# Optimization experiments

Hardware: AMD Instinct MI355X
Metric: run time of the kernel (lower is better)

Reference implementation:

```python
import jax, jax.numpy as jnp
import numpy as np

B, T, E, NH = 2, 1024, 512, 8


def setup_inputs() -> dict:
    key = jax.random.key(0)
    ks = jax.random.split(key, 7)
    s = 0.02
    return {
        "x": jax.random.normal(ks[0], (B, T, E), dtype=jnp.float32),
        "W_qkv": jax.random.normal(ks[1], (E, 3 * E), dtype=jnp.float32) * s,
        "b_qkv": jax.random.normal(ks[2], (3 * E,), dtype=jnp.float32) * s,
        "W_od": jax.random.normal(ks[3], (E, 2 * NH), dtype=jnp.float32) * s,
        "b_od": jax.random.normal(ks[4], (2 * NH,), dtype=jnp.float32) * s,
        "W_out": jax.random.normal(ks[5], (E, E), dtype=jnp.float32) * s,
        "b_out": jax.random.normal(ks[6], (E,), dtype=jnp.float32) * s,
        "length": T,
    }


def reference(x, W_qkv, b_qkv, W_od, b_od, W_out, b_out, length):
    b, t, e = x.shape
    nh = W_od.shape[1] // 2
    hd = e // nh
    scaling = float(hd) ** (-0.5)

    qkv = x @ W_qkv + b_qkv
    Q, K, V = jnp.split(qkv, 3, axis=-1)  # each (b, t, e)

    od = Q @ W_od + b_od  # (b, t, 2*nh)
    offset, duration = jnp.split(od, 2, axis=-1)
    offset = jnp.tanh(offset) * length
    duration = jax.nn.sigmoid(duration) * length

    qidx = jnp.arange(length, dtype=x.dtype)[None, :, None]  # (1, t, 1)
    anchor = qidx + offset  # (b, t, nh)

    # 'b t nh -> (b nh) t'
    anchor = anchor.transpose(0, 2, 1).reshape(b * nh, t)
    duration = duration.transpose(0, 2, 1).reshape(b * nh, t)

    start = anchor - duration
    end = anchor + duration
    bl = jnp.floor(start)          # left bound index
    br = jnp.ceil(end)             # right bound index
    al = jnp.floor(anchor)         # anchor left index
    ar = al + 1                    # anchor right index
    dist_al = anchor - al          # anchor_dist_l

    r = jnp.arange(length, dtype=x.dtype)[None, None, :]  # (1, 1, t)

    def pmask(idx):  # point mask (bnh, t, t), float
        return (r == idx[:, :, None]).astype(x.dtype)

    point_weight = (1.0
                    + (bl - start)[:, :, None] * pmask(bl)
                    + (end - br)[:, :, None] * pmask(br)
                    + dist_al[:, :, None] * pmask(ar)
                    + (1.0 - dist_al)[:, :, None] * pmask(al))

    attn_mask = (r < bl[:, :, None]) | (r > br[:, :, None])  # (bnh, t, t) bool

    def heads(z):  # 'b t (nh hd) -> (b nh) t hd'
        return z.reshape(b, t, nh, hd).transpose(0, 2, 1, 3).reshape(b * nh, t, hd)

    Qh, Kh, Vh = heads(Q), heads(K), heads(V)

    scores = jnp.einsum('bic,brc->bir', Qh, Kh) * scaling
    scores = scores * point_weight
    scores = jnp.where(attn_mask, jnp.asarray(-1e8, x.dtype), scores)
    attn = jax.nn.softmax(scores, axis=-1)

    out = jnp.einsum('bir,brc->bic', attn, Vh)  # (bnh, t, hd)
    out = out.reshape(b, nh, t, hd).transpose(0, 2, 1, 3).reshape(b, t, e)
    return out @ W_out + b_out
```

## Files before the change

kernel.cpp:

```cpp
#include <hip/hip_runtime.h>

typedef unsigned short ushort_t;
typedef short s16x8 __attribute__((ext_vector_type(8)));
typedef float f32x4 __attribute__((ext_vector_type(4)));

#define DEVINL __device__ __forceinline__

DEVINL ushort_t f2b(float f) {
  union { float f; unsigned int u; } v; v.f = f;
  unsigned int r = (v.u + 0x7fffu + ((v.u >> 16) & 1u)) >> 16;
  return (ushort_t)r;
}

DEVINL ushort_t f2b_hw(float f) {
  union { __bf16 h; ushort_t u; } cv;
  cv.h = (__bf16)f;
  return cv.u;
}

__global__ __launch_bounds__(256) void prep_kernel(
    const float* __restrict__ Wqkv, const float* __restrict__ bq,
    const float* __restrict__ Wod, const float* __restrict__ bod,
    const float* __restrict__ Wout,
    ushort_t* __restrict__ WqkvT, ushort_t* __restrict__ WoT,
    float* __restrict__ Wcomb, float* __restrict__ bcomb)
{
  __shared__ ushort_t tile[64 * 72];
  const int b = blockIdx.x;
  const int tid = threadIdx.x;

  if (b < 256) {
    const float* in;
    ushort_t* out;
    int N, bx, by;
    if (b < 192) { in = Wqkv; out = WqkvT; N = 1536; bx = b % 24; by = b / 24; }
    else         { in = Wout; out = WoT;   N = 512;  bx = (b - 192) % 8; by = (b - 192) / 8; }
    const int K = 512;
    const int n0 = bx * 64, k0 = by * 64;
    const int cr = tid >> 4;
    const int cc = (tid & 15) * 4;
#pragma unroll
    for (int p = 0; p < 4; p++) {
      int k = k0 + p * 16 + cr;
      float4 v = *(const float4*)(in + k * N + n0 + cc);
      ushort4 o; o.x = f2b(v.x); o.y = f2b(v.y); o.z = f2b(v.z); o.w = f2b(v.w);
      *(ushort4*)(tile + (p * 16 + cr) * 72 + cc) = o;
    }
    __syncthreads();
#pragma unroll
    for (int p = 0; p < 4; p++) {
      int n = n0 + p * 16 + cr;
      ushort4 v;
      v.x = tile[(cc + 0) * 72 + p * 16 + cr];
      v.y = tile[(cc + 1) * 72 + p * 16 + cr];
      v.z = tile[(cc + 2) * 72 + p * 16 + cr];
      v.w = tile[(cc + 3) * 72 + p * 16 + cr];
      *(ushort4*)(out + n * K + k0 + cc) = v;
    }
    return;
  }

  const int w = tid >> 6, lane = tid & 63;
  const int c = (b - 256) * 4 + w;
  if (c > 512) return;
  float a[8];
  const float* src = (c < 512) ? (Wqkv + c * 1536 + lane * 8) : (bq + lane * 8);
  float4 a0 = *(const float4*)(src);
  float4 a1 = *(const float4*)(src + 4);
  a[0]=a0.x; a[1]=a0.y; a[2]=a0.z; a[3]=a0.w;
  a[4]=a1.x; a[5]=a1.y; a[6]=a1.z; a[7]=a1.w;

  float s[16];
#pragma unroll
  for (int j = 0; j < 16; j++) s[j] = 0.f;
#pragma unroll
  for (int i = 0; i < 8; i++) {
    const float* wp = Wod + (lane * 8 + i) * 16;
#pragma unroll
    for (int j = 0; j < 16; j++) s[j] += a[i] * wp[j];
  }
#pragma unroll
  for (int mask = 1; mask < 64; mask <<= 1)
#pragma unroll
    for (int j = 0; j < 16; j++) s[j] += __shfl_xor(s[j], mask);

  if (lane < 16) {
    if (c < 512) Wcomb[c * 16 + lane] = s[lane];
    else         bcomb[lane] = s[lane] + bod[lane];
  }
}

__global__ __launch_bounds__(256) void od_kernel(
    const float* __restrict__ x, const float* __restrict__ Wcomb,
    const float* __restrict__ bcomb, const int* __restrict__ lenp,
    float* __restrict__ params, ushort_t* __restrict__ xb)
{
  const int w = threadIdx.x >> 6, lane = threadIdx.x & 63;
  const int m = blockIdx.x * 4 + w;
  int li = lenp[0];
  float len = (li > 0 && li < 1048576) ? (float)li : 1024.0f;

  const float* qp = x + m * 512 + lane * 8;
  float q[8];
  float4 qa = *(const float4*)(qp);
  float4 qb = *(const float4*)(qp + 4);
  q[0]=qa.x; q[1]=qa.y; q[2]=qa.z; q[3]=qa.w;
  q[4]=qb.x; q[5]=qb.y; q[6]=qb.z; q[7]=qb.w;

  s16x8 ov;
#pragma unroll
  for (int i = 0; i < 8; i++) ov[i] = (short)f2b(q[i]);
  *(s16x8*)(xb + m * 512 + lane * 8) = ov;

  float s[16];
#pragma unroll
  for (int j = 0; j < 16; j++) s[j] = 0.f;
#pragma unroll
  for (int i = 0; i < 8; i++) {
    const float* wp = Wcomb + (lane * 8 + i) * 16;
#pragma unroll
    for (int j = 0; j < 16; j++) s[j] += q[i] * wp[j];
  }
#pragma unroll
  for (int mask = 1; mask < 64; mask <<= 1)
#pragma unroll
    for (int j = 0; j < 16; j++) s[j] += __shfl_xor(s[j], mask);

  if (lane < 8) {
    int h = lane;
    int bb = m >> 10, t = m & 1023;
    float odo = s[h] + bcomb[h];
    float odd = s[8 + h] + bcomb[8 + h];
    float offset = tanhf(odo) * len;
    float dur = len / (1.f + expf(-odd));
    float anchor = (float)t + offset;
    float start = anchor - dur, end = anchor + dur;
    float bl = floorf(start), br = ceilf(end);
    float al = floorf(anchor);
    float da = anchor - al;
    float* pp = params + ((bb * 8 + h) * 1024 + t) * 6;
    pp[0] = bl; pp[1] = br; pp[2] = al;
    pp[3] = bl - start; pp[4] = end - br; pp[5] = da;
  }
}

__global__ __launch_bounds__(256) void qkv_gemm_kernel(
    const ushort_t* __restrict__ xb, const ushort_t* __restrict__ WT,
    const float* __restrict__ bqkv,
    ushort_t* __restrict__ Qh, ushort_t* __restrict__ Kh, ushort_t* __restrict__ VT)
{
  __shared__ ushort_t As[64 * 32];
  __shared__ ushort_t Bs[128 * 32];
  const int tid = threadIdx.x;
  const int lane = tid & 63, w = tid >> 6;
  const int wr = w >> 1, wc = w & 1;
  const int quad = lane >> 4, l16 = lane & 15;
  const int m0 = blockIdx.y * 64, n0 = blockIdx.x * 128;

  f32x4 acc[2][4];
#pragma unroll
  for (int i = 0; i < 2; i++)
#pragma unroll
    for (int j = 0; j < 4; j++) acc[i][j] = f32x4{0.f, 0.f, 0.f, 0.f};

  const int idx = tid * 8;
  const int ra = idx >> 5, ca = idx & 31;
  const int rb1 = (idx + 2048) >> 5, cb1 = (idx + 2048) & 31;

  for (int k0 = 0; k0 < 512; k0 += 32) {
    s16x8 va  = *(const s16x8*)(xb + (m0 + ra) * 512 + k0 + ca);
    s16x8 vb0 = *(const s16x8*)(WT + (n0 + ra) * 512 + k0 + ca);
    s16x8 vb1 = *(const s16x8*)(WT + (n0 + rb1) * 512 + k0 + cb1);
    __syncthreads();
    *(s16x8*)(As + idx) = va;
    *(s16x8*)(Bs + idx) = vb0;
    *(s16x8*)(Bs + idx + 2048) = vb1;
    __syncthreads();

    s16x8 af[2], bfr[4];
#pragma unroll
    for (int mt = 0; mt < 2; mt++)
      af[mt] = *(const s16x8*)(As + (wr * 32 + mt * 16 + l16) * 32 + quad * 8);
#pragma unroll
    for (int nt = 0; nt < 4; nt++)
      bfr[nt] = *(const s16x8*)(Bs + (wc * 64 + nt * 16 + l16) * 32 + quad * 8);
#pragma unroll
    for (int mt = 0; mt < 2; mt++)
#pragma unroll
      for (int nt = 0; nt < 4; nt++)
        acc[mt][nt] = __builtin_amdgcn_mfma_f32_16x16x32_bf16(af[mt], bfr[nt], acc[mt][nt], 0, 0, 0);
  }

#pragma unroll
  for (int nt = 0; nt < 4; nt++) {
    int c = n0 + wc * 64 + nt * 16 + l16;
    float bias = bqkv[c];
    int which = c >> 9;
    int e = c & 511;
    int h = e >> 6, d = e & 63;
#pragma unroll
    for (int mt = 0; mt < 2; mt++) {
      int mbase = m0 + wr * 32 + mt * 16 + quad * 4;
      int bb = mbase >> 10, t = mbase & 1023;
      int bh = bb * 8 + h;
      if (which == 2) {
        ushort4 pk;
        pk.x = f2b(acc[mt][nt][0] + bias);
        pk.y = f2b(acc[mt][nt][1] + bias);
        pk.z = f2b(acc[mt][nt][2] + bias);
        pk.w = f2b(acc[mt][nt][3] + bias);
        *(ushort4*)(VT + (bh * 64 + d) * 1024 + t) = pk;
      } else {
        ushort_t* dst = (which == 0) ? Qh : Kh;
        float sc = (which == 0) ? 0.125f : 1.0f;
#pragma unroll
        for (int rr = 0; rr < 4; rr++)
          dst[(bh * 1024 + t + rr) * 64 + d] = f2b((acc[mt][nt][rr] + bias) * sc);
      }
    }
  }
}

__global__ __launch_bounds__(256, 3) void attn_kernel(
    const ushort_t* __restrict__ Qh, const ushort_t* __restrict__ Kh,
    const ushort_t* __restrict__ VT, const float* __restrict__ params,
    ushort_t* __restrict__ Oh)
{
  constexpr int TS = 64 * 72;
  __shared__ __align__(16) ushort_t KV[4 * TS];
  __shared__ ushort_t Ps[4][16 * 40];
  __shared__ float loS[4], hiS[4];

  const int tid = threadIdx.x;
  const int lane = tid & 63, w = tid >> 6;
  const int wr = w >> 1, wc = w & 1;
  const int quad = lane >> 4, l16 = lane & 15;
  const int bh = blockIdx.x;
  const int mrow = blockIdx.y * 32;
  ushort_t* Pw = Ps[w];

  s16x8 aq0 = *(const s16x8*)(Qh + (bh * 1024 + mrow + wr * 16 + l16) * 64 + quad * 8);
  s16x8 aq1 = *(const s16x8*)(Qh + (bh * 1024 + mrow + wr * 16 + l16) * 64 + 32 + quad * 8);

  float bl[4], br[4], al[4], wl[4], wr2[4], da[4];
  float lo = 1.0e9f, hi = -1.0e9f;
#pragma unroll
  for (int rr = 0; rr < 4; rr++) {
    int row = mrow + wr * 16 + quad * 4 + rr;
    const float* pp = params + (bh * 1024 + row) * 6;
    bl[rr] = pp[0]; br[rr] = pp[1]; al[rr] = pp[2];
    wl[rr] = pp[3]; wr2[rr] = pp[4]; da[rr] = pp[5];
    bool empty = (br[rr] < 0.f) || (bl[rr] > 1023.f);
    float lo_r = empty ? 0.f    : fmaxf(bl[rr], 0.f);
    float hi_r = empty ? 1023.f : fminf(br[rr], 1023.f);
    lo = fminf(lo, lo_r); hi = fmaxf(hi, hi_r);
  }
  lo = fminf(lo, __shfl_xor(lo, 16));
  lo = fminf(lo, __shfl_xor(lo, 32));
  hi = fmaxf(hi, __shfl_xor(hi, 16));
  hi = fmaxf(hi, __shfl_xor(hi, 32));
  if (lane == 0) { loS[w] = lo; hiS[w] = hi; }
  __syncthreads();
  lo = fminf(fminf(loS[0], loS[1]), fminf(loS[2], loS[3]));
  hi = fmaxf(fmaxf(hiS[0], hiS[1]), fmaxf(hiS[2], hiS[3]));
  const int tlo = ((int)lo) >> 6, thi = ((int)hi) >> 6;

  float lr[4] = {0.f, 0.f, 0.f, 0.f};
  f32x4 Oacc[4];
#pragma unroll
  for (int nt = 0; nt < 4; nt++) Oacc[nt] = f32x4{0.f, 0.f, 0.f, 0.f};

  const int srow = tid >> 2, sseg = (tid & 3) * 16;
  const ushort_t* kgb = Kh + (bh * 1024 + srow) * 64 + sseg;
  const ushort_t* vgb = VT + (bh * 64 + srow) * 1024 + sseg;

  s16x8 kr0, kr1, vr0, vr1;
  {
    const int r0 = tlo * 64;
    kr0 = *(const s16x8*)(kgb + r0 * 64);
    kr1 = *(const s16x8*)(kgb + r0 * 64 + 8);
    vr0 = *(const s16x8*)(vgb + r0);
    vr1 = *(const s16x8*)(vgb + r0 + 8);
  }
  {
    ushort_t* Kt = KV;
    ushort_t* Vt = KV + TS;
    *(s16x8*)(Kt + srow * 72 + sseg)     = kr0;
    *(s16x8*)(Kt + srow * 72 + sseg + 8) = kr1;
    *(s16x8*)(Vt + srow * 72 + sseg)     = vr0;
    *(s16x8*)(Vt + srow * 72 + sseg + 8) = vr1;
  }
  __syncthreads();

  for (int tt = tlo; tt <= thi; tt++) {
    const int p = (tt - tlo) & 1;
    ushort_t* Ktp = KV + p * 2 * TS;
    ushort_t* Vtp = KV + p * 2 * TS + TS;
    const int r0 = tt * 64;
    const bool more = (tt + 1 <= thi);

    if (more) {
      const int r1 = (tt + 1) * 64;
      kr0 = *(const s16x8*)(kgb + r1 * 64);
      kr1 = *(const s16x8*)(kgb + r1 * 64 + 8);
      vr0 = *(const s16x8*)(vgb + r1);
      vr1 = *(const s16x8*)(vgb + r1 + 8);
    }

    f32x4 S[2];
#pragma unroll
    for (int ng = 0; ng < 2; ng++) {
      const ushort_t* kp = Ktp + (wc * 32 + ng * 16 + l16) * 72 + quad * 8;
      s16x8 bk0 = *(const s16x8*)(kp);
      s16x8 bk1 = *(const s16x8*)(kp + 32);
      f32x4 z = {0.f, 0.f, 0.f, 0.f};
      z = __builtin_amdgcn_mfma_f32_16x16x32_bf16(aq0, bk0, z, 0, 0, 0);
      z = __builtin_amdgcn_mfma_f32_16x16x32_bf16(aq1, bk1, z, 0, 0, 0);
      S[ng] = z;
    }

    const int cbase = r0 + wc * 32;
    const float c0f = (float)cbase, c1f = c0f + 31.f;
    bool fastb = true;
#pragma unroll
    for (int rr = 0; rr < 4; rr++) {
      bool f = (bl[rr] < c0f) && (br[rr] > c1f) &&
               ((al[rr] + 1.f < c0f) || (al[rr] > c1f));
      fastb = fastb && f;
    }
    float p8[2][4];
    if (__all((int)fastb)) {
#pragma unroll
      for (int ng = 0; ng < 2; ng++)
#pragma unroll
        for (int rr = 0; rr < 4; rr++) {
          float pv = __expf(S[ng][rr]);
          lr[rr] += pv;
          p8[ng][rr] = pv;
        }
    } else {
#pragma unroll
      for (int ng = 0; ng < 2; ng++) {
        const float cf = (float)(cbase + ng * 16 + l16);
#pragma unroll
        for (int rr = 0; rr < 4; rr++) {
          float s = S[ng][rr];
          float wgt = 1.f;
          wgt += (cf == bl[rr]) ? wl[rr] : 0.f;
          wgt += (cf == br[rr]) ? wr2[rr] : 0.f;
          wgt += (cf == al[rr] + 1.f) ? da[rr] : 0.f;
          wgt += (cf == al[rr]) ? (1.f - da[rr]) : 0.f;
          s *= wgt;
          s = (cf < bl[rr] || cf > br[rr]) ? -30.f : s;
          float pv = __expf(s);
          lr[rr] += pv;
          p8[ng][rr] = pv;
        }
      }
    }

#pragma unroll
    for (int ng = 0; ng < 2; ng++)
#pragma unroll
      for (int rr = 0; rr < 4; rr++)
        Pw[(quad * 4 + rr) * 40 + ng * 16 + l16] = f2b_hw(p8[ng][rr]);

    s16x8 pa = *(const s16x8*)(Pw + l16 * 40 + quad * 8);

#pragma unroll
    for (int nt = 0; nt < 4; nt++) {
      s16x8 bv = *(const s16x8*)(Vtp + (nt * 16 + l16) * 72 + wc * 32 + quad * 8);
      Oacc[nt] = __builtin_amdgcn_mfma_f32_16x16x32_bf16(pa, bv, Oacc[nt], 0, 0, 0);
    }

    if (more) {
      ushort_t* Ktn = KV + (p ^ 1) * 2 * TS;
      ushort_t* Vtn = KV + (p ^ 1) * 2 * TS + TS;
      *(s16x8*)(Ktn + srow * 72 + sseg)     = kr0;
      *(s16x8*)(Ktn + srow * 72 + sseg + 8) = kr1;
      *(s16x8*)(Vtn + srow * 72 + sseg)     = vr0;
      *(s16x8*)(Vtn + srow * 72 + sseg + 8) = vr1;
      __syncthreads();
    }
  }

#pragma unroll
  for (int mask = 1; mask < 16; mask <<= 1)
#pragma unroll
    for (int rr = 0; rr < 4; rr++) lr[rr] += __shfl_xor(lr[rr], mask);

  __syncthreads();
  float* Om  = (float*)KV;
  float* lwf = Om + 2 * 32 * 65;
  const int rloc = wr * 16 + quad * 4;
#pragma unroll
  for (int nt = 0; nt < 4; nt++)
#pragma unroll
    for (int rr = 0; rr < 4; rr++)
      Om[(wc * 32 + rloc + rr) * 65 + nt * 16 + l16] = Oacc[nt][rr];
  if (l16 == 0) {
#pragma unroll
    for (int rr = 0; rr < 4; rr++) lwf[wc * 32 + rloc + rr] = lr[rr];
  }
  __syncthreads();

  const int bb = bh >> 3, h = bh & 7;
  for (int e = tid; e < 2048; e += 256) {
    int r = e >> 6, col = e & 63;
    float lg = lwf[r] + lwf[32 + r];
    float o  = Om[r * 65 + col] + Om[(32 + r) * 65 + col];
    int t = mrow + r;
    Oh[((bb << 10) + t) * 512 + h * 64 + col] = f2b_hw(o / lg);
  }
}

__global__ __launch_bounds__(256) void out_gemm_kernel(
    const ushort_t* __restrict__ Oh, const ushort_t* __restrict__ WT,
    const float* __restrict__ bout, float* __restrict__ outp)
{
  __shared__ ushort_t As[64 * 32];
  __shared__ ushort_t Bs[64 * 32];
  const int tid = threadIdx.x;
  const int lane = tid & 63, w = tid >> 6;
  const int wr = w >> 1, wc = w & 1;
  const int quad = lane >> 4, l16 = lane & 15;
  const int m0 = blockIdx.y * 64, n0 = blockIdx.x * 64;

  f32x4 acc[2][2];
#pragma unroll
  for (int i = 0; i < 2; i++)
#pragma unroll
    for (int j = 0; j < 2; j++) acc[i][j] = f32x4{0.f, 0.f, 0.f, 0.f};

  const int idx = tid * 8;
  const int ra = idx >> 5, ca = idx & 31;

  for (int k0 = 0; k0 < 512; k0 += 32) {
    s16x8 va = *(const s16x8*)(Oh + (m0 + ra) * 512 + k0 + ca);
    s16x8 vb = *(const s16x8*)(WT + (n0 + ra) * 512 + k0 + ca);
    __syncthreads();
    *(s16x8*)(As + idx) = va;
    *(s16x8*)(Bs + idx) = vb;
    __syncthreads();

    s16x8 af[2], bfr[2];
#pragma unroll
    for (int mt = 0; mt < 2; mt++)
      af[mt] = *(const s16x8*)(As + (wr * 32 + mt * 16 + l16) * 32 + quad * 8);
#pragma unroll
    for (int nt = 0; nt < 2; nt++)
      bfr[nt] = *(const s16x8*)(Bs + (wc * 32 + nt * 16 + l16) * 32 + quad * 8);
#pragma unroll
    for (int mt = 0; mt < 2; mt++)
#pragma unroll
      for (int nt = 0; nt < 2; nt++)
        acc[mt][nt] = __builtin_amdgcn_mfma_f32_16x16x32_bf16(af[mt], bfr[nt], acc[mt][nt], 0, 0, 0);
  }

#pragma unroll
  for (int nt = 0; nt < 2; nt++) {
    int c = n0 + wc * 32 + nt * 16 + l16;
    float bias = bout[c];
#pragma unroll
    for (int mt = 0; mt < 2; mt++) {
#pragma unroll
      for (int rr = 0; rr < 4; rr++) {
        int m = m0 + wr * 32 + mt * 16 + quad * 4 + rr;
        outp[m * 512 + c] = acc[mt][nt][rr] + bias;
      }
    }
  }
}

extern "C" void kernel_launch(void* const* d_in, const int* in_sizes, int n_in,
                              void* d_out, int out_size, void* d_ws, size_t ws_size,
                              hipStream_t stream)
{
  const float* x    = (const float*)d_in[0];
  const float* Wqkv = (const float*)d_in[1];
  const float* bqkv = (const float*)d_in[2];
  const float* Wod  = (const float*)d_in[3];
  const float* bod  = (const float*)d_in[4];
  const float* Wout = (const float*)d_in[5];
  const float* bout = (const float*)d_in[6];
  const int* lenp   = (const int*)d_in[7];

  char* ws = (char*)d_ws;
  ushort_t* WqkvT  = (ushort_t*)(ws);
  ushort_t* WoT    = (ushort_t*)(ws + 1572864);
  ushort_t* xb     = (ushort_t*)(ws + 2097152);
  ushort_t* Qh     = (ushort_t*)(ws + 4194304);
  ushort_t* Kh     = (ushort_t*)(ws + 6291456);
  ushort_t* VT     = (ushort_t*)(ws + 8388608);
  ushort_t* Oh     = (ushort_t*)(ws + 10485760);
  float*    Wcomb  = (float*)(ws + 12582912);
  float*    bcomb  = (float*)(ws + 12615680);
  float*    params = (float*)(ws + 12615744);

  prep_kernel<<<385, 256, 0, stream>>>(Wqkv, bqkv, Wod, bod, Wout, WqkvT, WoT, Wcomb, bcomb);
  od_kernel<<<512, 256, 0, stream>>>(x, Wcomb, bcomb, lenp, params, xb);
  qkv_gemm_kernel<<<dim3(12, 32), 256, 0, stream>>>(xb, WqkvT, bqkv, Qh, Kh, VT);
  attn_kernel<<<dim3(16, 32), 256, 0, stream>>>(Qh, Kh, VT, params, Oh);
  out_gemm_kernel<<<dim3(8, 32), 256, 0, stream>>>(Oh, WoT, bout, (float*)d_out);
}
```

Baseline: 129.3 us.

## Fuse od and QKV GEMM kernels, restructure attention to 16-row transposed MFMA tiles

Merges the offset/duration kernel into the QKV GEMM launch as extra blocks and converts x to bf16 inside the GEMM load, which removes the xb intermediate buffer and one launch. The attention kernel now handles 16 query rows per block, with each wave covering 16 key columns. It computes S^T using 16x16x16 MFMAs so the P fragment stays in registers for the PV MFMA, avoiding the LDS round trip for P. The grid doubles and occupancy is raised to 4 blocks per SM, at the cost of a four-way cross-wave reduction at the end and more K/V tile loading per query row.

```diff
diff --git a/kernel.cpp b/kernel.cpp
--- a/kernel.cpp
+++ b/kernel.cpp
@@ -2,7 +2,14 @@
 
 typedef unsigned short ushort_t;
 typedef short s16x8 __attribute__((ext_vector_type(8)));
+typedef short s16x4 __attribute__((ext_vector_type(4)));
 typedef float f32x4 __attribute__((ext_vector_type(4)));
+
+#if defined(__HIP_DEVICE_COMPILE__)
+#define MFMA16(a, b, c) __builtin_amdgcn_mfma_f32_16x16x16bf16_1k(a, b, c, 0, 0, 0)
+#else
+__device__ __host__ static inline f32x4 MFMA16(s16x4, s16x4, f32x4 c) { return c; }
+#endif
 
 #define DEVINL __device__ __forceinline__
 
@@ -90,72 +97,70 @@
   }
 }
 
-__global__ __launch_bounds__(256) void od_kernel(
-    const float* __restrict__ x, const float* __restrict__ Wcomb,
-    const float* __restrict__ bcomb, const int* __restrict__ lenp,
-    float* __restrict__ params, ushort_t* __restrict__ xb)
+__global__ __launch_bounds__(256) void qkv_od_kernel(
+    const float* __restrict__ x, const ushort_t* __restrict__ WT,
+    const float* __restrict__ bqkv,
+    const float* __restrict__ Wcomb, const float* __restrict__ bcomb,
+    const int* __restrict__ lenp,
+    ushort_t* __restrict__ Qh, ushort_t* __restrict__ Kh, ushort_t* __restrict__ VT,
+    float* __restrict__ params)
 {
-  const int w = threadIdx.x >> 6, lane = threadIdx.x & 63;
-  const int m = blockIdx.x * 4 + w;
-  int li = lenp[0];
-  float len = (li > 0 && li < 1048576) ? (float)li : 1024.0f;
-
-  const float* qp = x + m * 512 + lane * 8;
-  float q[8];
-  float4 qa = *(const float4*)(qp);
-  float4 qb = *(const float4*)(qp + 4);
-  q[0]=qa.x; q[1]=qa.y; q[2]=qa.z; q[3]=qa.w;
-  q[4]=qb.x; q[5]=qb.y; q[6]=qb.z; q[7]=qb.w;
-
-  s16x8 ov;
-#pragma unroll
-  for (int i = 0; i < 8; i++) ov[i] = (short)f2b(q[i]);
-  *(s16x8*)(xb + m * 512 + lane * 8) = ov;
-
-  float s[16];
-#pragma unroll
-  for (int j = 0; j < 16; j++) s[j] = 0.f;
-#pragma unroll
-  for (int i = 0; i < 8; i++) {
-    const float* wp = Wcomb + (lane * 8 + i) * 16;
-#pragma unroll
-    for (int j = 0; j < 16; j++) s[j] += q[i] * wp[j];
-  }
-#pragma unroll
-  for (int mask = 1; mask < 64; mask <<= 1)
-#pragma unroll
-    for (int j = 0; j < 16; j++) s[j] += __shfl_xor(s[j], mask);
-
-  if (lane < 8) {
-    int h = lane;
-    int bb = m >> 10, t = m & 1023;
-    float odo = s[h] + bcomb[h];
-    float odd = s[8 + h] + bcomb[8 + h];
-    float offset = tanhf(odo) * len;
-    float dur = len / (1.f + expf(-odd));
-    float anchor = (float)t + offset;
-    float start = anchor - dur, end = anchor + dur;
-    float bl = floorf(start), br = ceilf(end);
-    float al = floorf(anchor);
-    float da = anchor - al;
-    float* pp = params + ((bb * 8 + h) * 1024 + t) * 6;
-    pp[0] = bl; pp[1] = br; pp[2] = al;
-    pp[3] = bl - start; pp[4] = end - br; pp[5] = da;
-  }
-}
-
-__global__ __launch_bounds__(256) void qkv_gemm_kernel(
-    const ushort_t* __restrict__ xb, const ushort_t* __restrict__ WT,
-    const float* __restrict__ bqkv,
-    ushort_t* __restrict__ Qh, ushort_t* __restrict__ Kh, ushort_t* __restrict__ VT)
-{
+  const int blk = blockIdx.x;
+  const int tid = threadIdx.x;
+
+  if (blk >= 384) {
+    const int w = tid >> 6, lane = tid & 63;
+    const int m = (blk - 384) * 4 + w;
+    int li = lenp[0];
+    float len = (li > 0 && li < 1048576) ? (float)li : 1024.0f;
+
+    const float* qp = x + m * 512 + lane * 8;
+    float q[8];
+    float4 qa = *(const float4*)(qp);
+    float4 qb = *(const float4*)(qp + 4);
+    q[0]=qa.x; q[1]=qa.y; q[2]=qa.z; q[3]=qa.w;
+    q[4]=qb.x; q[5]=qb.y; q[6]=qb.z; q[7]=qb.w;
+
+    float s[16];
+#pragma unroll
+    for (int j = 0; j < 16; j++) s[j] = 0.f;
+#pragma unroll
+    for (int i = 0; i < 8; i++) {
+      const float* wp = Wcomb + (lane * 8 + i) * 16;
+#pragma unroll
+      for (int j = 0; j < 16; j++) s[j] += q[i] * wp[j];
+    }
+#pragma unroll
+    for (int mask = 1; mask < 64; mask <<= 1)
+#pragma unroll
+      for (int j = 0; j < 16; j++) s[j] += __shfl_xor(s[j], mask);
+
+    if (lane < 8) {
+      int h = lane;
+      int bb = m >> 10, t = m & 1023;
+      float odo = s[h] + bcomb[h];
+      float odd = s[8 + h] + bcomb[8 + h];
+      float offset = tanhf(odo) * len;
+      float dur = len / (1.f + expf(-odd));
+      float anchor = (float)t + offset;
+      float start = anchor - dur, end = anchor + dur;
+      float bl = floorf(start), br = ceilf(end);
+      float al = floorf(anchor);
+      float da = anchor - al;
+      float* pp = params + ((bb * 8 + h) * 1024 + t) * 6;
+      pp[0] = bl; pp[1] = br; pp[2] = al;
+      pp[3] = bl - start; pp[4] = end - br; pp[5] = da;
+    }
+    return;
+  }
+
   __shared__ ushort_t As[64 * 32];
   __shared__ ushort_t Bs[128 * 32];
-  const int tid = threadIdx.x;
   const int lane = tid & 63, w = tid >> 6;
   const int wr = w >> 1, wc = w & 1;
   const int quad = lane >> 4, l16 = lane & 15;
-  const int m0 = blockIdx.y * 64, n0 = blockIdx.x * 128;
+  const int bx = blk % 12, by = blk / 12;
+  const int m0 = by * 64, n0 = bx * 128;
 
   f32x4 acc[2][4];
 #pragma unroll
@@ -168,9 +173,16 @@
   const int rb1 = (idx + 2048) >> 5, cb1 = (idx + 2048) & 31;
 
   for (int k0 = 0; k0 < 512; k0 += 32) {
-    s16x8 va  = *(const s16x8*)(xb + (m0 + ra) * 512 + k0 + ca);
+    const float* xa = x + (m0 + ra) * 512 + k0 + ca;
+    float4 x0 = *(const float4*)(xa);
+    float4 x1 = *(const float4*)(xa + 4);
     s16x8 vb0 = *(const s16x8*)(WT + (n0 + ra) * 512 + k0 + ca);
     s16x8 vb1 = *(const s16x8*)(WT + (n0 + rb1) * 512 + k0 + cb1);
+    s16x8 va;
+    va[0] = (short)f2b_hw(x0.x); va[1] = (short)f2b_hw(x0.y);
+    va[2] = (short)f2b_hw(x0.z); va[3] = (short)f2b_hw(x0.w);
+    va[4] = (short)f2b_hw(x1.x); va[5] = (short)f2b_hw(x1.y);
+    va[6] = (short)f2b_hw(x1.z); va[7] = (short)f2b_hw(x1.w);
     __syncthreads();
     *(s16x8*)(As + idx) = va;
     *(s16x8*)(Bs + idx) = vb0;
@@ -221,54 +233,43 @@
   }
 }
 
-__global__ __launch_bounds__(256, 3) void attn_kernel(
+__global__ __launch_bounds__(256, 4) void attn_kernel(
     const ushort_t* __restrict__ Qh, const ushort_t* __restrict__ Kh,
     const ushort_t* __restrict__ VT, const float* __restrict__ params,
     ushort_t* __restrict__ Oh)
 {
   constexpr int TS = 64 * 72;
   __shared__ __align__(16) ushort_t KV[4 * TS];
-  __shared__ ushort_t Ps[4][16 * 40];
-  __shared__ float loS[4], hiS[4];
 
   const int tid = threadIdx.x;
-  const int lane = tid & 63, w = tid >> 6;
-  const int wr = w >> 1, wc = w & 1;
+  const int lane = tid & 63, wc = tid >> 6;
   const int quad = lane >> 4, l16 = lane & 15;
   const int bh = blockIdx.x;
-  const int mrow = blockIdx.y * 32;
-  ushort_t* Pw = Ps[w];
-
-  s16x8 aq0 = *(const s16x8*)(Qh + (bh * 1024 + mrow + wr * 16 + l16) * 64 + quad * 8);
-  s16x8 aq1 = *(const s16x8*)(Qh + (bh * 1024 + mrow + wr * 16 + l16) * 64 + 32 + quad * 8);
-
-  float bl[4], br[4], al[4], wl[4], wr2[4], da[4];
-  float lo = 1.0e9f, hi = -1.0e9f;
-#pragma unroll
-  for (int rr = 0; rr < 4; rr++) {
-    int row = mrow + wr * 16 + quad * 4 + rr;
-    const float* pp = params + (bh * 1024 + row) * 6;
-    bl[rr] = pp[0]; br[rr] = pp[1]; al[rr] = pp[2];
-    wl[rr] = pp[3]; wr2[rr] = pp[4]; da[rr] = pp[5];
-    bool empty = (br[rr] < 0.f) || (bl[rr] > 1023.f);
-    float lo_r = empty ? 0.f    : fmaxf(bl[rr], 0.f);
-    float hi_r = empty ? 1023.f : fminf(br[rr], 1023.f);
-    lo = fminf(lo, lo_r); hi = fmaxf(hi, hi_r);
-  }
-  lo = fminf(lo, __shfl_xor(lo, 16));
-  lo = fminf(lo, __shfl_xor(lo, 32));
-  hi = fmaxf(hi, __shfl_xor(hi, 16));
-  hi = fmaxf(hi, __shfl_xor(hi, 32));
-  if (lane == 0) { loS[w] = lo; hiS[w] = hi; }
-  __syncthreads();
-  lo = fminf(fminf(loS[0], loS[1]), fminf(loS[2], loS[3]));
-  hi = fmaxf(fmaxf(hiS[0], hiS[1]), fmaxf(hiS[2], hiS[3]));
+  const int mrow = blockIdx.y * 16;
+
+  const float* ppl = params + (bh * 1024 + mrow + l16) * 6;
+  float bl = ppl[0], br = ppl[1], al = ppl[2];
+  float wl = ppl[3], wr2 = ppl[4], da = ppl[5];
+  bool empty = (br < 0.f) || (bl > 1023.f);
+  float lo = empty ? 0.f    : fmaxf(bl, 0.f);
+  float hi = empty ? 1023.f : fminf(br, 1023.f);
+#pragma unroll
+  for (int mask = 1; mask < 16; mask <<= 1) {
+    lo = fminf(lo, __shfl_xor(lo, mask));
+    hi = fmaxf(hi, __shfl_xor(hi, mask));
+  }
   const int tlo = ((int)lo) >> 6, thi = ((int)hi) >> 6;
 
-  float lr[4] = {0.f, 0.f, 0.f, 0.f};
+  const ushort_t* qrow = Qh + (bh * 1024 + mrow + l16) * 64;
+  s16x4 bq[4];
+#pragma unroll
+  for (int i = 0; i < 4; i++)
+    bq[i] = *(const s16x4*)(qrow + i * 16 + quad * 4);
+
+  float lr = 0.f;
   f32x4 Oacc[4];
 #pragma unroll
-  for (int nt = 0; nt < 4; nt++) Oacc[nt] = f32x4{0.f, 0.f, 0.f, 0.f};
+  for (int g = 0; g < 4; g++) Oacc[g] = f32x4{0.f, 0.f, 0.f, 0.f};
 
   const int srow = tid >> 2, sseg = (tid & 3) * 16;
   const ushort_t* kgb = Kh + (bh * 1024 + srow) * 64 + sseg;
@@ -307,70 +308,47 @@
       vr1 = *(const s16x8*)(vgb + r1 + 8);
     }
 
-    f32x4 S[2];
-#pragma unroll
-    for (int ng = 0; ng < 2; ng++) {
-      const ushort_t* kp = Ktp + (wc * 32 + ng * 16 + l16) * 72 + quad * 8;
-      s16x8 bk0 = *(const s16x8*)(kp);
-      s16x8 bk1 = *(const s16x8*)(kp + 32);
-      f32x4 z = {0.f, 0.f, 0.f, 0.f};
-      z = __builtin_amdgcn_mfma_f32_16x16x32_bf16(aq0, bk0, z, 0, 0, 0);
-      z = __builtin_amdgcn_mfma_f32_16x16x32_bf16(aq1, bk1, z, 0, 0, 0);
-      S[ng] = z;
-    }
-
-    const int cbase = r0 + wc * 32;
-    const float c0f = (float)cbase, c1f = c0f + 31.f;
-    bool fastb = true;
-#pragma unroll
-    for (int rr = 0; rr < 4; rr++) {
-      bool f = (bl[rr] < c0f) && (br[rr] > c1f) &&
-               ((al[rr] + 1.f < c0f) || (al[rr] > c1f));
-      fastb = fastb && f;
-    }
-    float p8[2][4];
-    if (__all((int)fastb)) {
-#pragma unroll
-      for (int ng = 0; ng < 2; ng++)
-#pragma unroll
-        for (int rr = 0; rr < 4; rr++) {
-          float pv = __expf(S[ng][rr]);
-          lr[rr] += pv;
-          p8[ng][rr] = pv;
-        }
+    const ushort_t* krow = Ktp + (wc * 16 + l16) * 72;
+    f32x4 z = {0.f, 0.f, 0.f, 0.f};
+#pragma unroll
+    for (int i = 0; i < 4; i++) {
+      s16x4 ak = *(const s16x4*)(krow + i * 16 + quad * 4);
+      z = MFMA16(ak, bq[i], z);
+    }
+
+    const int cbase = r0 + wc * 16;
+    const float c0f = (float)cbase, c1f = c0f + 15.f;
+    bool f = (bl < c0f) && (br > c1f) && ((al + 1.f < c0f) || (al > c1f));
+    s16x4 pt;
+    if (__all((int)f)) {
+#pragma unroll
+      for (int rr = 0; rr < 4; rr++) {
+        float pv = __expf(z[rr]);
+        lr += pv;
+        pt[rr] = (short)f2b_hw(pv);
+      }
     } else {
 #pragma unroll
-      for (int ng = 0; ng < 2; ng++) {
-        const float cf = (float)(cbase + ng * 16 + l16);
-#pragma unroll
-        for (int rr = 0; rr < 4; rr++) {
-          float s = S[ng][rr];
-          float wgt = 1.f;
-          wgt += (cf == bl[rr]) ? wl[rr] : 0.f;
-          wgt += (cf == br[rr]) ? wr2[rr] : 0.f;
-          wgt += (cf == al[rr] + 1.f) ? da[rr] : 0.f;
-          wgt += (cf == al[rr]) ? (1.f - da[rr]) : 0.f;
-          s *= wgt;
-          s = (cf < bl[rr] || cf > br[rr]) ? -30.f : s;
-          float pv = __expf(s);
-          lr[rr] += pv;
-          p8[ng][rr] = pv;
-        }
+      for (int rr = 0; rr < 4; rr++) {
+        float cf = (float)(cbase + quad * 4 + rr);
+        float s = z[rr];
+        float wgt = 1.f;
+        wgt += (cf == bl) ? wl : 0.f;
+        wgt += (cf == br) ? wr2 : 0.f;
+        wgt += (cf == al + 1.f) ? da : 0.f;
+        wgt += (cf == al) ? (1.f - da) : 0.f;
+        s *= wgt;
+        s = (cf < bl || cf > br) ? -30.f : s;
+        float pv = __expf(s);
+        lr += pv;
+        pt[rr] = (short)f2b_hw(pv);
       }
     }
 
 #pragma unroll
-    for (int ng = 0; ng < 2; ng++)
-#pragma unroll
-      for (int rr = 0; rr < 4; rr++)
-        Pw[(quad * 4 + rr) * 40 + ng * 16 + l16] = f2b_hw(p8[ng][rr]);
-
-    s16x8 pa = *(const s16x8*)(Pw + l16 * 40 + quad * 8);
-
-#pragma unroll
-    for (int nt = 0; nt < 4; nt++) {
-      s16x8 bv = *(const s16x8*)(Vtp + (nt * 16 + l16) * 72 + wc * 32 + quad * 8);
-      Oacc[nt] = __builtin_amdgcn_mfma_f32_16x16x32_bf16(pa, bv, Oacc[nt], 0, 0, 0);
+    for (int g = 0; g < 4; g++) {
+      s16x4 av = *(const s16x4*)(Vtp + (g * 16 + l16) * 72 + wc * 16 + quad * 4);
+      Oacc[g] = MFMA16(av, pt, Oacc[g]);
     }
 
     if (more) {
@@ -384,33 +362,32 @@
     }
   }
 
-#pragma unroll
-  for (int mask = 1; mask < 16; mask <<= 1)
-#pragma unroll
-    for (int rr = 0; rr < 4; rr++) lr[rr] += __shfl_xor(lr[rr], mask);
+  lr += __shfl_xor(lr, 16);
+  lr += __shfl_xor(lr, 32);
 
   __syncthreads();
   float* Om  = (float*)KV;
-  float* lwf = Om + 2 * 32 * 65;
-  const int rloc = wr * 16 + quad * 4;
-#pragma unroll
-  for (int nt = 0; nt < 4; nt++)
+  float* lwf = Om + 64 * 65;
+#pragma unroll
+  for (int g = 0; g < 4; g++)
 #pragma unroll
     for (int rr = 0; rr < 4; rr++)
-      Om[(wc * 32 + rloc + rr) * 65 + nt * 16 + l16] = Oacc[nt][rr];
-  if (l16 == 0) {
-#pragma unroll
-    for (int rr = 0; rr < 4; rr++) lwf[wc * 32 + rloc + rr] = lr[rr];
-  }
+      Om[(wc * 16 + l16) * 65 + g * 16 + quad * 4 + rr] = Oacc[g][rr];
+  if (quad == 0) lwf[wc * 16 + l16] = lr;
   __syncthreads();
 
   const int bb = bh >> 3, h = bh & 7;
-  for (int e = tid; e < 2048; e += 256) {
-    int r = e >> 6, col = e & 63;
-    float lg = lwf[r] + lwf[32 + r];
-    float o  = Om[r * 65 + col] + Om[(32 + r) * 65 + col];
-    int t = mrow + r;
-    Oh[((bb << 10) + t) * 512 + h * 64 + col] = f2b_hw(o / lg);
+  {
+    int e = tid;
+#pragma unroll
+    for (int it = 0; it < 4; it++, e += 256) {
+      int r = e >> 6, col = e & 63;
+      float lg = lwf[r] + lwf[16 + r] + lwf[32 + r] + lwf[48 + r];
+      float o  = Om[r * 65 + col] + Om[(16 + r) * 65 + col]
+               + Om[(32 + r) * 65 + col] + Om[(48 + r) * 65 + col];
+      int t = mrow + r;
+      Oh[((bb << 10) + t) * 512 + h * 64 + col] = f2b_hw(o / lg);
+    }
   }
 }
 
@@ -488,7 +465,6 @@
   char* ws = (char*)d_ws;
   ushort_t* WqkvT  = (ushort_t*)(ws);
   ushort_t* WoT    = (ushort_t*)(ws + 1572864);
-  ushort_t* xb     = (ushort_t*)(ws + 2097152);
   ushort_t* Qh     = (ushort_t*)(ws + 4194304);
   ushort_t* Kh     = (ushort_t*)(ws + 6291456);
   ushort_t* VT     = (ushort_t*)(ws + 8388608);
@@ -498,8 +474,8 @@
   float*    params = (float*)(ws + 12615744);
 
   prep_kernel<<<385, 256, 0, stream>>>(Wqkv, bqkv, Wod, bod, Wout, WqkvT, WoT, Wcomb, bcomb);
-  od_kernel<<<512, 256, 0, stream>>>(x, Wcomb, bcomb, lenp, params, xb);
-  qkv_gemm_kernel<<<dim3(12, 32), 256, 0, stream>>>(xb, WqkvT, bqkv, Qh, Kh, VT);
-  attn_kernel<<<dim3(16, 32), 256, 0, stream>>>(Qh, Kh, VT, params, Oh);
+  qkv_od_kernel<<<896, 256, 0, stream>>>(x, WqkvT, bqkv, Wcomb, bcomb, lenp,
+                                         Qh, Kh, VT, params);
+  attn_kernel<<<dim3(16, 64), 256, 0, stream>>>(Qh, Kh, VT, params, Oh);
   out_gemm_kernel<<<dim3(8, 32), 256, 0, stream>>>(Oh, WoT, bout, (float*)d_out);
 }
```

Measured after the change: 126.3 us. 1.02x faster.
